# Optimization experiments

Hardware: AMD Instinct MI355X
Metric: run time of the kernel (lower is better)

Reference implementation:

```python
import jax, jax.numpy as jnp
import numpy as np

N, C, H, W = 8, 32, 16, 16   # input batch / channels / spatial
OC = 64                       # out_channels
K = 3                         # kernel_size
PAD = 1                       # padding (stride=1, dilation=1 -> output HxW == input HxW)
WIDTH = 8                     # hwcfg['width']
RLEN = 2 ** WIDTH             # Sobol RNG sequence length = 256
CKK = C * K * K               # unfolded patch length = 288
B = N * H * W                 # flattened patch batch = 2048


def _sobol_rng():
    # 1-D Sobol sequence == van der Corput base-2: bit-reversed counter scaled to [0, 2^width)
    idx = np.arange(RLEN, dtype=np.uint32)
    rev = np.zeros(RLEN, dtype=np.uint32)
    for b in range(WIDTH):
        rev |= ((idx >> b) & 1) << (WIDTH - 1 - b)
    return jnp.asarray(rev.astype(np.float32))


def setup_inputs() -> dict:
    key = jax.random.key(0)
    k1, k2, k3, k4, k5, k6 = jax.random.split(key, 6)
    # unary (stochastic bitstream) input: bits in {0,1}
    x = jax.random.bernoulli(k1, 0.5, (N, C, H, W)).astype(jnp.float32)
    # BinGen, bipolar: binary = round((v + 1)/2 * 2^width), v in [-1, 1]
    w = jax.random.uniform(k2, (OC, CKK), minval=-1.0, maxval=1.0)
    w_bin = jnp.round((w + 1.0) / 2.0 * RLEN)
    b = jax.random.uniform(k3, (OC,), minval=-1.0, maxval=1.0)
    b_bin = jnp.round((b + 1.0) / 2.0 * RLEN)
    rng = _sobol_rng()
    # mid-stream BSGen index state (per patch position, as the module cats to batch copies)
    wrdx_i1 = jax.random.randint(k4, (B, OC, CKK), 0, RLEN, dtype=jnp.int32)
    wrdx_i0 = jax.random.randint(k5, (B, OC, CKK), 0, RLEN, dtype=jnp.int32)
    brdx = jax.random.randint(k6, (OC,), 0, RLEN, dtype=jnp.int32)
    return {"x": x, "w_bin": w_bin, "b_bin": b_bin, "rng": rng,
            "wrdx_i1": wrdx_i1, "wrdx_i0": wrdx_i0, "brdx": brdx}


def _unfold(x):
    # even cycle -> ConstantPad2d(pad, 0); torch.nn.functional.unfold ordering (c, kh, kw)
    xp = jnp.pad(x, ((0, 0), (0, 0), (PAD, PAD), (PAD, PAD)))
    cols = jnp.stack([xp[:, :, i:i + H, j:j + W] for i in range(K) for j in range(K)], axis=2)
    # [N, C, K*K, H, W] -> [N, CKK, L] -> [N, L, CKK] -> [B, CKK]
    return cols.reshape(N, CKK, H * W).transpose(0, 2, 1).reshape(B, CKK)


def reference(x, w_bin, b_bin, rng, wrdx_i1, wrdx_i0, brdx):
    ib1 = _unfold(x)                                                        # [B, CKK], bits
    # BSGen: bit = (binary_value > rng[index % RLEN])
    wbit1 = (w_bin[None] > rng[wrdx_i1 % RLEN]).astype(jnp.float32)         # [B, OC, CKK]
    wbit0 = 1.0 - (w_bin[None] > rng[wrdx_i0 % RLEN]).astype(jnp.float32)   # [B, OC, CKK]
    # bipolar parallel counter: x*w1 path + (1-x)*(1-w) path
    obin = (jnp.einsum('bk,bok->bo', ib1, wbit1)
            + jnp.einsum('bk,bok->bo', 1.0 - ib1, wbit0))                   # [B, OC]
    bbit = (b_bin > rng[brdx % RLEN]).astype(jnp.float32)                   # [OC]
    # fold(1,1): [N, L, OC] -> [N, OC, H, W]
    out = obin.reshape(N, H * W, OC).transpose(0, 2, 1).reshape(N, OC, H, W)
    return out + bbit[None, :, None, None]
```

## Files before the change

kernel.cpp:

```cpp
#include <hip/hip_runtime.h>


#define CH   32
#define HH   16
#define WW   16
#define OCN  64
#define CKK  288
#define LL   256
#define BB   2048

__device__ __forceinline__ float sobol_val(int idx) {
    return (float)(__brev((unsigned)idx) >> 24);
}

__device__ __forceinline__ float contrib(float xb, float wv, int i1, int i0) {
    float t1  = (wv > sobol_val(i1)) ? 1.f : 0.f;
    float nt0 = (wv > sobol_val(i0)) ? 0.f : 1.f;
    return (xb != 0.f) ? t1 : nt0;
}

__device__ __forceinline__ int4 ntload(const int4* p) {
    typedef __attribute__((ext_vector_type(4))) int i4;
    i4 v = __builtin_nontemporal_load((const i4*)p);
    return make_int4(v.x, v.y, v.z, v.w);
}

__global__ __launch_bounds__(256) void fsuconv_kernel(
    const float* __restrict__ x,
    const float* __restrict__ w_bin,
    const float* __restrict__ b_bin,
    const int*   __restrict__ wrdx1,
    const int*   __restrict__ wrdx0,
    const int*   __restrict__ brdx,
    float*       __restrict__ out)
{
    __shared__ __align__(16) float ib1[CKK];

    const int blk = blockIdx.x;
    const int b   = blk >> 4;
    const int og  = blk & 15;
    const int n   = b >> 8;
    const int l   = b & 255;
    const int h   = l >> 4;
    const int w0  = l & 15;

    for (int k = threadIdx.x; k < CKK; k += 256) {
        int c  = k / 9;
        int r  = k - c * 9;
        int kh = r / 3;
        int kw = r - kh * 3;
        int ih = h + kh - 1;
        int iw = w0 + kw - 1;
        float v = 0.f;
        if ((unsigned)ih < 16u && (unsigned)iw < 16u)
            v = x[((n * CH + c) * HH + ih) * WW + iw];
        ib1[k] = v;
    }
    __syncthreads();

    const int wave = threadIdx.x >> 6;
    const int lane = threadIdx.x & 63;
    const int o    = og * 4 + wave;

    const size_t rowoff = ((size_t)b * OCN + o) * CKK;
    const int4*   r1 = (const int4*)(wrdx1 + rowoff);
    const int4*   r0 = (const int4*)(wrdx0 + rowoff);
    const float4* wr = (const float4*)(w_bin + (size_t)o * CKK);

    float sum = 0.f;

    {
        int4   a  = ntload(&r1[lane]);
        int4   c0 = ntload(&r0[lane]);
        float4 wv = wr[lane];
        float4 xv = *(const float4*)&ib1[lane * 4];
        sum += contrib(xv.x, wv.x, a.x, c0.x);
        sum += contrib(xv.y, wv.y, a.y, c0.y);
        sum += contrib(xv.z, wv.z, a.z, c0.z);
        sum += contrib(xv.w, wv.w, a.w, c0.w);
    }
    if (lane < 8) {
        int4   a  = ntload(&r1[64 + lane]);
        int4   c0 = ntload(&r0[64 + lane]);
        float4 wv = wr[64 + lane];
        float4 xv = *(const float4*)&ib1[256 + lane * 4];
        sum += contrib(xv.x, wv.x, a.x, c0.x);
        sum += contrib(xv.y, wv.y, a.y, c0.y);
        sum += contrib(xv.z, wv.z, a.z, c0.z);
        sum += contrib(xv.w, wv.w, a.w, c0.w);
    }

    for (int off = 32; off > 0; off >>= 1)
        sum += __shfl_down(sum, off);

    if (lane == 0) {
        float bb = (b_bin[o] > sobol_val(brdx[o])) ? 1.f : 0.f;
        out[((size_t)n * OCN + o) * LL + l] = sum + bb;
    }
}

extern "C" void kernel_launch(void* const* d_in, const int* in_sizes, int n_in,
                              void* d_out, int out_size, void* d_ws, size_t ws_size,
                              hipStream_t stream) {
    const float* x     = (const float*)d_in[0];
    const float* w_bin = (const float*)d_in[1];
    const float* b_bin = (const float*)d_in[2];
    const int*   wrdx1 = (const int*)d_in[4];
    const int*   wrdx0 = (const int*)d_in[5];
    const int*   brdx  = (const int*)d_in[6];
    float*       out   = (float*)d_out;

    dim3 grid(BB * 16);
    dim3 block(256);
    fsuconv_kernel<<<grid, block, 0, stream>>>(x, w_bin, b_bin, wrdx1, wrdx0, brdx, out);
}
```

Before: 310.7 us.

## Replace float compare-and-reduce with ballot bitmasks and popcount, two outputs per wave

Each comparison result is turned into a wave-wide bitmask with ballot. Counts come from popcount, which removes the shuffle reduction. The weight comparison is done as an unsigned integer compare against the bit-reversed index, with no int-to-float conversion. Each wave now handles two output channels and the grid is halved, so more independent loads are in flight per wave. The tail lanes load duplicate data and are masked out. The kernel is memory-bound on the large index arrays, so the gain from the extra ALU savings may be limited.

Measured after the change: 298.7 us, median of 2. 1.04x faster.

```diff
diff --git a/kernel.cpp b/kernel.cpp
--- a/kernel.cpp
+++ b/kernel.cpp
@@ -13,16 +13,22 @@
     return (float)(__brev((unsigned)idx) >> 24);
 }
 
-__device__ __forceinline__ float contrib(float xb, float wv, int i1, int i0) {
-    float t1  = (wv > sobol_val(i1)) ? 1.f : 0.f;
-    float nt0 = (wv > sobol_val(i0)) ? 0.f : 1.f;
-    return (xb != 0.f) ? t1 : nt0;
+__device__ __forceinline__ unsigned wkeyf(float wv) {
+    unsigned wi = (unsigned)wv;
+    return (wi >= 256u) ? 0xFFFFFFFFu : (wi << 24);
 }
 
 __device__ __forceinline__ int4 ntload(const int4* p) {
     typedef __attribute__((ext_vector_type(4))) int i4;
     i4 v = __builtin_nontemporal_load((const i4*)p);
     return make_int4(v.x, v.y, v.z, v.w);
+}
+
+__device__ __forceinline__ unsigned long long chunkm(unsigned k, int a1, int a0,
+                                                     unsigned long long xm) {
+    unsigned long long m1 = __ballot(k > __brev((unsigned)a1));
+    unsigned long long m0 = __ballot(k > __brev((unsigned)a0));
+    return (xm & m1) | (~xm & ~m0);
 }
 
 __global__ __launch_bounds__(256) void fsuconv_kernel(
@@ -37,8 +43,8 @@
     __shared__ __align__(16) float ib1[CKK];
 
     const int blk = blockIdx.x;
-    const int b   = blk >> 4;
-    const int og  = blk & 15;
+    const int b   = blk >> 3;
+    const int og  = blk & 7;
     const int n   = b >> 8;
     const int l   = b & 255;
     const int h   = l >> 4;
@@ -60,42 +66,67 @@
 
     const int wave = threadIdx.x >> 6;
     const int lane = threadIdx.x & 63;
-    const int o    = og * 4 + wave;
+    const int tl   = 64 + (lane & 7);
 
-    const size_t rowoff = ((size_t)b * OCN + o) * CKK;
-    const int4*   r1 = (const int4*)(wrdx1 + rowoff);
-    const int4*   r0 = (const int4*)(wrdx0 + rowoff);
-    const float4* wr = (const float4*)(w_bin + (size_t)o * CKK);
+    float4 xv = ((const float4*)ib1)[lane];
+    float4 xt = ((const float4*)ib1)[tl];
+    const unsigned long long x0 = __ballot(xv.x != 0.f);
+    const unsigned long long x1 = __ballot(xv.y != 0.f);
+    const unsigned long long x2 = __ballot(xv.z != 0.f);
+    const unsigned long long x3 = __ballot(xv.w != 0.f);
+    const unsigned long long y0 = __ballot(xt.x != 0.f);
+    const unsigned long long y1 = __ballot(xt.y != 0.f);
+    const unsigned long long y2 = __ballot(xt.z != 0.f);
+    const unsigned long long y3 = __ballot(xt.w != 0.f);
 
-    float sum = 0.f;
+    const int oA = og * 8 + wave * 2;
+    const int oB = oA + 1;
+    const size_t offA = ((size_t)b * OCN + oA) * CKK;
+    const size_t offB = ((size_t)b * OCN + oB) * CKK;
+
+    const int4* r1A = (const int4*)(wrdx1 + offA);
+    const int4* r0A = (const int4*)(wrdx0 + offA);
+    const int4* r1B = (const int4*)(wrdx1 + offB);
+    const int4* r0B = (const int4*)(wrdx0 + offB);
+    const float4* wA = (const float4*)(w_bin + (size_t)oA * CKK);
+    const float4* wB = (const float4*)(w_bin + (size_t)oB * CKK);
+
+    int4 aA  = ntload(&r1A[lane]);   int4 cA  = ntload(&r0A[lane]);
+    int4 aB  = ntload(&r1B[lane]);   int4 cB  = ntload(&r0B[lane]);
+    int4 aAt = ntload(&r1A[tl]);     int4 cAt = ntload(&r0A[tl]);
+    int4 aBt = ntload(&r1B[tl]);     int4 cBt = ntload(&r0B[tl]);
+    float4 wvA = wA[lane];           float4 wtA = wA[tl];
+    float4 wvB = wB[lane];           float4 wtB = wB[tl];
 
     {
-        int4   a  = ntload(&r1[lane]);
-        int4   c0 = ntload(&r0[lane]);
-        float4 wv = wr[lane];
-        float4 xv = *(const float4*)&ib1[lane * 4];
-        sum += contrib(xv.x, wv.x, a.x, c0.x);
-        sum += contrib(xv.y, wv.y, a.y, c0.y);
-        sum += contrib(xv.z, wv.z, a.z, c0.z);
-        sum += contrib(xv.w, wv.w, a.w, c0.w);
+        unsigned cnt = 0;
+        cnt += __popcll(chunkm(wkeyf(wvA.x), aA.x,  cA.x,  x0));
+        cnt += __popcll(chunkm(wkeyf(wvA.y), aA.y,  cA.y,  x1));
+        cnt += __popcll(chunkm(wkeyf(wvA.z), aA.z,  cA.z,  x2));
+        cnt += __popcll(chunkm(wkeyf(wvA.w), aA.w,  cA.w,  x3));
+        cnt += __popcll(chunkm(wkeyf(wtA.x), aAt.x, cAt.x, y0) & 0xFFull);
+        cnt += __popcll(chunkm(wkeyf(wtA.y), aAt.y, cAt.y, y1) & 0xFFull);
+        cnt += __popcll(chunkm(wkeyf(wtA.z), aAt.z, cAt.z, y2) & 0xFFull);
+        cnt += __popcll(chunkm(wkeyf(wtA.w), aAt.w, cAt.w, y3) & 0xFFull);
+        if (lane == 0) {
+            float bb = (b_bin[oA] > sobol_val(brdx[oA])) ? 1.f : 0.f;
+            out[((size_t)n * OCN + oA) * LL + l] = (float)cnt + bb;
+        }
     }
-    if (lane < 8) {
-        int4   a  = ntload(&r1[64 + lane]);
-        int4   c0 = ntload(&r0[64 + lane]);
-        float4 wv = wr[64 + lane];
-        float4 xv = *(const float4*)&ib1[256 + lane * 4];
-        sum += contrib(xv.x, wv.x, a.x, c0.x);
-        sum += contrib(xv.y, wv.y, a.y, c0.y);
-        sum += contrib(xv.z, wv.z, a.z, c0.z);
-        sum += contrib(xv.w, wv.w, a.w, c0.w);
-    }
-
-    for (int off = 32; off > 0; off >>= 1)
-        sum += __shfl_down(sum, off);
-
-    if (lane == 0) {
-        float bb = (b_bin[o] > sobol_val(brdx[o])) ? 1.f : 0.f;
-        out[((size_t)n * OCN + o) * LL + l] = sum + bb;
+    {
+        unsigned cnt = 0;
+        cnt += __popcll(chunkm(wkeyf(wvB.x), aB.x,  cB.x,  x0));
+        cnt += __popcll(chunkm(wkeyf(wvB.y), aB.y,  cB.y,  x1));
+        cnt += __popcll(chunkm(wkeyf(wvB.z), aB.z,  cB.z,  x2));
+        cnt += __popcll(chunkm(wkeyf(wvB.w), aB.w,  cB.w,  x3));
+        cnt += __popcll(chunkm(wkeyf(wtB.x), aBt.x, cBt.x, y0) & 0xFFull);
+        cnt += __popcll(chunkm(wkeyf(wtB.y), aBt.y, cBt.y, y1) & 0xFFull);
+        cnt += __popcll(chunkm(wkeyf(wtB.z), aBt.z, cBt.z, y2) & 0xFFull);
+        cnt += __popcll(chunkm(wkeyf(wtB.w), aBt.w, cBt.w, y3) & 0xFFull);
+        if (lane == 0) {
+            float bb = (b_bin[oB] > sobol_val(brdx[oB])) ? 1.f : 0.f;
+            out[((size_t)n * OCN + oB) * LL + l] = (float)cnt + bb;
+        }
     }
 }
 
@@ -110,7 +141,7 @@
     const int*   brdx  = (const int*)d_in[6];
     float*       out   = (float*)d_out;
 
-    dim3 grid(BB * 16);
+    dim3 grid(BB * 8);
     dim3 block(256);
     fsuconv_kernel<<<grid, block, 0, stream>>>(x, w_bin, b_bin, wrdx1, wrdx0, brdx, out);
 }
```
